# Kernel optimization log

Hardware: AMD Instinct MI355X
Metric: run time of the kernel (lower is better)

The kernel has to match this reference:

```python
import jax, jax.numpy as jnp
import numpy as np

B, A, IN, H, NA = 256, 32, 512, 512, 64


def setup_inputs() -> dict:
    key = jax.random.key(0)
    ks = jax.random.split(key, 9)
    s = 1.0 / np.sqrt(H).astype(np.float32)
    si = 1.0 / np.sqrt(IN).astype(np.float32)
    return {
        "inputs": jax.random.normal(ks[0], (B * A, IN), jnp.float32),
        "hidden_state": jnp.zeros((B, A, H), jnp.float32),
        "W1": jax.random.normal(ks[1], (A, H, IN), jnp.float32) * si,
        "b1": jax.random.normal(ks[2], (A, H), jnp.float32) * si,
        "W_ih": jax.random.normal(ks[3], (A, 3 * H, H), jnp.float32) * s,
        "b_ih": jax.random.normal(ks[4], (A, 3 * H), jnp.float32) * s,
        "W_hh": jax.random.normal(ks[5], (A, 3 * H, H), jnp.float32) * s,
        "b_hh": jax.random.normal(ks[6], (A, 3 * H), jnp.float32) * s,
        "W2": jax.random.normal(ks[7], (A, NA, H), jnp.float32) * s,
        "b2": jax.random.normal(ks[8], (A, NA), jnp.float32) * s,
    }


def reference(inputs, hidden_state, W1, b1, W_ih, b_ih, W_hh, b_hh, W2, b2):
    # inputs: [B*A, IN] -> [B, A, IN]; per-agent distinct weights stacked on axis 0 (a)
    x = inputs.reshape(-1, A, IN)
    h_in = hidden_state  # [B, A, H]
    # fc1 + relu, grouped over agents
    x1 = jax.nn.relu(jnp.einsum('bai,ahi->bah', x, W1) + b1)
    # GRUCell (PyTorch gate layout: r, z, n)
    gx = jnp.einsum('bah,agh->bag', x1, W_ih) + b_ih   # [B, A, 3H]
    gh = jnp.einsum('bah,agh->bag', h_in, W_hh) + b_hh  # [B, A, 3H]
    gx_r, gx_z, gx_n = jnp.split(gx, 3, axis=-1)
    gh_r, gh_z, gh_n = jnp.split(gh, 3, axis=-1)
    r = jax.nn.sigmoid(gx_r + gh_r)
    z = jax.nn.sigmoid(gx_z + gh_z)
    n = jnp.tanh(gx_n + r * gh_n)
    h = (1.0 - z) * n + z * h_in  # [B, A, H]
    # fc2 per agent
    q = jnp.einsum('bah,anh->ban', h, W2) + b2  # [B, A, NA]
    # torch: cat(qs, dim=-1).view(-1, n_actions) == reshape to [B*A, NA]
    return q.reshape(-1, NA), h
```

## Files before the change

kernel.cpp:

```cpp
#include <hip/hip_runtime.h>
#include <hip/hip_bf16.h>


typedef __attribute__((ext_vector_type(8))) __bf16 bf16x8;
typedef __attribute__((ext_vector_type(4))) float  f32x4;

constexpr int NAGENT = 32;
constexpr int KC     = 512;

__device__ __forceinline__ bf16x8 cvt8(const float* p) {
  f32x4 u = *(const f32x4*)p;
  f32x4 v = *(const f32x4*)(p + 4);
  bf16x8 w;
  w[0] = (__bf16)u[0]; w[1] = (__bf16)u[1]; w[2] = (__bf16)u[2]; w[3] = (__bf16)u[3];
  w[4] = (__bf16)v[0]; w[5] = (__bf16)v[1]; w[6] = (__bf16)v[2]; w[7] = (__bf16)v[3];
  return w;
}
__device__ __forceinline__ float sigmoid_f(float x) { return 1.f / (1.f + __expf(-x)); }
__device__ __forceinline__ float tanh_f(float x) {
  float xc = fminf(fmaxf(x, -15.f), 15.f);
  float a = __expf(2.f * xc);
  return (a - 1.f) / (a + 1.f);
}
__device__ __forceinline__ int xcd_swz(int bid, int nwg) {
  return (bid & 7) * (nwg >> 3) + (bid >> 3);
}


__global__ __launch_bounds__(256) void prep_k(
    const float* __restrict__ hidden, __bf16* __restrict__ AF) {
  const int idx = blockIdx.x * 256 + threadIdx.x;
  const int kc = idx & 63;
  const int row = idx >> 6;
  const int a = row & 31, b = row >> 5;
  bf16x8 v = cvt8(hidden + (size_t)row * KC + kc * 8);
  *(bf16x8*)(AF + ((size_t)(a * 128 + 64 + kc) * 256 + b) * 8) = v;
}

__global__ __launch_bounds__(512, 2) void fc1_k(
    const float* __restrict__ inputs, const float* __restrict__ W1,
    const float* __restrict__ b1, __bf16* __restrict__ AF) {
  const int wg = xcd_swz(blockIdx.x, gridDim.x);
  const int a  = wg >> 3;
  const int n0 = (wg & 7) * 64;

  __shared__ __attribute__((aligned(16))) __bf16 lA[2][256][8][8];
  __shared__ __attribute__((aligned(16))) __bf16 lB[2][64][8][8];

  const int tid = threadIdx.x;
  const int lane = tid & 63;
  const int wave = tid >> 6;
  const int wm = wave >> 1, wn = wave & 1;
  const int lr = lane & 15, lk = lane >> 4;

  int arow[4], aks[4]; size_t aoff[4];
#pragma unroll
  for (int c = 0; c < 4; ++c) {
    const int idx = c * 512 + tid;
    arow[c] = idx >> 3; aks[c] = idx & 7;
    aoff[c] = ((size_t)arow[c] * NAGENT + a) * KC + aks[c] * 8;
  }
  const int brow = tid >> 3, bks = tid & 7;
  const size_t boff = ((size_t)a * 512 + n0 + brow) * KC + bks * 8;

  bf16x8 sA[4], sB;
  auto loadT = [&](int t) {
    const int kb = t * 64;
#pragma unroll
    for (int c = 0; c < 4; ++c) sA[c] = cvt8(inputs + aoff[c] + kb);
    sB = cvt8(W1 + boff + kb);
  };
  auto writeT = [&](int buf) {
#pragma unroll
    for (int c = 0; c < 4; ++c)
      *(bf16x8*)(&lA[buf][arow[c]][aks[c] ^ (arow[c] & 7)][0]) = sA[c];
    *(bf16x8*)(&lB[buf][brow][bks ^ (brow & 7)][0]) = sB;
  };

  f32x4 acc[4][2] = {};
  auto computeT = [&](int buf) {
#pragma unroll
    for (int s = 0; s < 2; ++s) {
      const int ks = s * 4 + lk;
      bf16x8 af[4];
#pragma unroll
      for (int i = 0; i < 4; ++i) {
        const int row = wm * 64 + i * 16 + lr;
        af[i] = *(const bf16x8*)(&lA[buf][row][ks ^ (row & 7)][0]);
      }
#pragma unroll
      for (int cb = 0; cb < 2; ++cb) {
        const int br = wn * 32 + cb * 16 + lr;
        bf16x8 bv = *(const bf16x8*)(&lB[buf][br][ks ^ (br & 7)][0]);
#pragma unroll
        for (int i = 0; i < 4; ++i)
          acc[i][cb] = __builtin_amdgcn_mfma_f32_16x16x32_bf16(af[i], bv, acc[i][cb], 0, 0, 0);
      }
    }
  };

  loadT(0); writeT(0);
  int cur = 0;
#pragma unroll 1
  for (int t = 0; t < 8; ++t) {
    __syncthreads();
    if (t < 7) loadT(t + 1);
    computeT(cur);
    if (t < 7) { writeT(cur ^ 1); cur ^= 1; }
  }

#pragma unroll
  for (int cb = 0; cb < 2; ++cb) {
    const int col = n0 + wn * 32 + cb * 16 + lr;
    const int kc = col >> 3, c7 = col & 7;
    const float bias = b1[(size_t)a * 512 + col];
#pragma unroll
    for (int i = 0; i < 4; ++i) {
      const int r0 = wm * 64 + i * 16 + lk * 4;
#pragma unroll
      for (int e = 0; e < 4; ++e) {
        const float v = fmaxf(acc[i][cb][e] + bias, 0.f);
        AF[((size_t)(a * 128 + kc) * 256 + r0 + e) * 8 + c7] = (__bf16)v;
      }
    }
  }
}

__global__ __launch_bounds__(1024, 4) void gru_k(
    const __bf16* __restrict__ AF,
    const float* __restrict__ Wih, const float* __restrict__ bih,
    const float* __restrict__ Whh, const float* __restrict__ bhh,
    float* __restrict__ hout, __bf16* __restrict__ hbf) {
  const int wg = xcd_swz(blockIdx.x, gridDim.x);
  const int a  = wg >> 3;
  const int n0 = (wg & 7) * 64;

  __shared__ __attribute__((aligned(16))) __bf16 lB[2][192][8][8];

  const int tid = threadIdx.x;
  const int lane = tid & 63;
  const int wave = tid >> 6;
  const int wm = wave >> 1;
  const int wc = wave & 1;
  const int lr = lane & 15, lk = lane >> 4;

  const int br0 = tid >> 3, bks = tid & 7;
  const int br1 = 128 + (tid >> 3);
  auto wrow = [&](int r) {
    return (size_t)a * 1536 + (r >> 6) * 512 + n0 + (r & 63);
  };
  const size_t boff0 = wrow(br0) * KC + bks * 8;
  const size_t boff1 = (tid < 512 ? wrow(br1) * KC + bks * 8 : 0);

  size_t aBase[2];
#pragma unroll
  for (int i = 0; i < 2; ++i)
    aBase[i] = (size_t)a * 262144 + (size_t)lk * 2048 +
               (size_t)(wm * 32 + i * 16 + lr) * 8;

  bf16x8 sB0, sB1;
  auto loadB = [&](int t) {
    const float* W = (t < 8) ? Wih : Whh;
    const int kb = (t & 7) * 64;
    sB0 = cvt8(W + boff0 + kb);
    if (tid < 512) sB1 = cvt8(W + boff1 + kb);
  };
  auto writeB = [&](int buf) {
    *(bf16x8*)(&lB[buf][br0][bks ^ (br0 & 7)][0]) = sB0;
    if (tid < 512) *(bf16x8*)(&lB[buf][br1][bks ^ (br1 & 7)][0]) = sB1;
  };

  f32x4 accR[2][2] = {}, accZ[2][2] = {}, accXN[2][2] = {}, accHN[2][2] = {};
  auto compute = [&](int buf, int t, f32x4 (&accN)[2][2]) {
    bf16x8 af[2][2];
#pragma unroll
    for (int s = 0; s < 2; ++s)
#pragma unroll
      for (int i = 0; i < 2; ++i)
        af[s][i] = *(const bf16x8*)(AF + aBase[i] + (size_t)t * 16384 + s * 8192);
#pragma unroll
    for (int s = 0; s < 2; ++s) {
      const int ks = s * 4 + lk;
#pragma unroll
      for (int cc = 0; cc < 2; ++cc) {
        const int rr = wc * 32 + cc * 16 + lr;
        const int sw = ks ^ (rr & 7);
        bf16x8 bR = *(const bf16x8*)(&lB[buf][rr][sw][0]);
        bf16x8 bZ = *(const bf16x8*)(&lB[buf][64 + rr][sw][0]);
        bf16x8 bN = *(const bf16x8*)(&lB[buf][128 + rr][sw][0]);
#pragma unroll
        for (int i = 0; i < 2; ++i) {
          accR[i][cc] = __builtin_amdgcn_mfma_f32_16x16x32_bf16(af[s][i], bR, accR[i][cc], 0, 0, 0);
          accZ[i][cc] = __builtin_amdgcn_mfma_f32_16x16x32_bf16(af[s][i], bZ, accZ[i][cc], 0, 0, 0);
          accN[i][cc] = __builtin_amdgcn_mfma_f32_16x16x32_bf16(af[s][i], bN, accN[i][cc], 0, 0, 0);
        }
      }
    }
  };

  loadB(0); writeB(0);
  int cur = 0;
#pragma unroll 1
  for (int t = 0; t < 8; ++t) {
    __syncthreads();
    loadB(t + 1);
    compute(cur, t, accXN);
    writeB(cur ^ 1); cur ^= 1;
  }
#pragma unroll 1
  for (int t = 8; t < 16; ++t) {
    __syncthreads();
    if (t < 15) loadB(t + 1);
    compute(cur, t, accHN);
    if (t < 15) { writeB(cur ^ 1); cur ^= 1; }
  }

#pragma unroll
  for (int cc = 0; cc < 2; ++cc) {
    const int col = n0 + wc * 32 + cc * 16 + lr;
    const size_t ab = (size_t)a * 1536 + col;
    const float br_ = bih[ab] + bhh[ab];
    const float bz_ = bih[ab + 512] + bhh[ab + 512];
    const float bxn = bih[ab + 1024];
    const float bhn = bhh[ab + 1024];
    const size_t hfb = ((size_t)(a * 128 + 64 + (col >> 3)) * 256) * 8 + (col & 7);
#pragma unroll
    for (int i = 0; i < 2; ++i) {
      const int r0 = wm * 32 + i * 16 + lk * 4;
#pragma unroll
      for (int e = 0; e < 4; ++e) {
        const float hprev = (float)AF[hfb + (size_t)(r0 + e) * 8];
        const float r = sigmoid_f(accR[i][cc][e] + br_);
        const float z = sigmoid_f(accZ[i][cc][e] + bz_);
        const float n = tanh_f((accXN[i][cc][e] + bxn) + r * (accHN[i][cc][e] + bhn));
        const float h = (1.f - z) * n + z * hprev;
        const size_t o = ((size_t)(r0 + e) * NAGENT + a) * KC + col;
        hout[o] = h;
        hbf[o] = (__bf16)h;
      }
    }
  }
}

template <bool ABF16, int ACT, bool OBF16>
__global__ __launch_bounds__(256) void gemm64(
    const void* __restrict__ Ap, const float* __restrict__ Wp,
    const float* __restrict__ bp, void* __restrict__ Op, const int N) {
  constexpr int BM = 64, MT = 4;
  const int NT = N >> 6;
  const int wg = xcd_swz(blockIdx.x, gridDim.x);
  const int a  = wg / (MT * NT);
  const int rem = wg % (MT * NT);
  const int n0 = (rem / MT) * 64;
  const int b0 = (rem % MT) * BM;

  __shared__ __attribute__((aligned(16))) __bf16 lA[2][4][64][8];
  __shared__ __attribute__((aligned(16))) __bf16 lB[2][4][64][8];

  const int tid = threadIdx.x;
  const int lane = tid & 63;
  const int wn = tid >> 6;
  const int lr = lane & 15, lk = lane >> 4;

  const int ar = tid >> 2, aks = tid & 3;
  const size_t aoff = ((size_t)(b0 + ar) * NAGENT + a) * KC + aks * 8;
  const size_t boff = ((size_t)a * N + n0 + ar) * KC + aks * 8;

  const float*  Af = (const float*)Ap;
  const __bf16* Ab = (const __bf16*)Ap;

  bf16x8 sA, sB;
  auto loadT = [&](int t) {
    if constexpr (ABF16) sA = *(const bf16x8*)(Ab + aoff + t * 32);
    else                 sA = cvt8(Af + aoff + t * 32);
    sB = cvt8(Wp + boff + t * 32);
  };
  auto writeT = [&](int buf) {
    *(bf16x8*)(&lA[buf][aks][ar][0]) = sA;
    *(bf16x8*)(&lB[buf][aks][ar][0]) = sB;
  };

  f32x4 acc[4] = {};
  auto computeT = [&](int buf) {
    bf16x8 bv = *(const bf16x8*)(&lB[buf][lk][wn * 16 + lr][0]);
#pragma unroll
    for (int i = 0; i < 4; ++i) {
      bf16x8 af = *(const bf16x8*)(&lA[buf][lk][i * 16 + lr][0]);
      acc[i] = __builtin_amdgcn_mfma_f32_16x16x32_bf16(af, bv, acc[i], 0, 0, 0);
    }
  };

  loadT(0); writeT(0);
  int cur = 0;
#pragma unroll 1
  for (int t = 0; t < KC / 32; ++t) {
    __syncthreads();
    if (t + 1 < KC / 32) loadT(t + 1);
    computeT(cur);
    if (t + 1 < KC / 32) { writeT(cur ^ 1); cur ^= 1; }
  }

  const int col = n0 + wn * 16 + lr;
  const float bias = bp[(size_t)a * N + col];
#pragma unroll
  for (int i = 0; i < 4; ++i) {
    const int r0 = b0 + i * 16 + lk * 4;
#pragma unroll
    for (int e = 0; e < 4; ++e) {
      float v = acc[i][e] + bias;
      if (ACT == 1) v = fmaxf(v, 0.f);
      const size_t o = ((size_t)(r0 + e) * NAGENT + a) * N + col;
      if constexpr (OBF16) ((__bf16*)Op)[o] = (__bf16)v;
      else                 ((float*)Op)[o]  = v;
    }
  }
}

extern "C" void kernel_launch(void* const* d_in, const int* in_sizes, int n_in,
                              void* d_out, int out_size, void* d_ws, size_t ws_size,
                              hipStream_t stream) {
  const float* inputs = (const float*)d_in[0];
  const float* hidden = (const float*)d_in[1];
  const float* W1   = (const float*)d_in[2];
  const float* b1   = (const float*)d_in[3];
  const float* W_ih = (const float*)d_in[4];
  const float* b_ih = (const float*)d_in[5];
  const float* W_hh = (const float*)d_in[6];
  const float* b_hh = (const float*)d_in[7];
  const float* W2   = (const float*)d_in[8];
  const float* b2   = (const float*)d_in[9];

  float* out_q = (float*)d_out;
  float* out_h = out_q + (size_t)8192 * 64;

  char* ws = (char*)d_ws;
  __bf16* AF  = (__bf16*)(ws);
  __bf16* hbf = (__bf16*)(ws + ((size_t)16 << 20));

  prep_k<<<2048, 256, 0, stream>>>(hidden, AF);
  fc1_k<<<256, 512, 0, stream>>>(inputs, W1, b1, AF);
  gru_k<<<256, 1024, 0, stream>>>(AF, W_ih, b_ih, W_hh, b_hh, out_h, hbf);
  gemm64<true, 0, false><<<128, 256, 0, stream>>>(hbf, W2, b2, out_q, 64);
}
```

Before: 112.7 us.

## Deepen GRU gate GEMM pipeline with two-ahead B prefetch and A register double-buffer

The GRU gate GEMM loop now prefetches weight tiles two steps ahead into two register sets and double-buffers the A fragments in registers, loading the next step's A before computing the current one. The barrier moves to after the LDS write, and both loops are fully unrolled. The goal is to hide global-load latency behind MFMA work. In exchange it raises VGPR pressure, which may reduce occupancy, and the full unroll grows code size.

```diff
diff --git a/kernel.cpp b/kernel.cpp
--- a/kernel.cpp
+++ b/kernel.cpp
@@ -158,26 +158,29 @@
     aBase[i] = (size_t)a * 262144 + (size_t)lk * 2048 +
                (size_t)(wm * 32 + i * 16 + lr) * 8;
 
-  bf16x8 sB0, sB1;
-  auto loadB = [&](int t) {
+  bf16x8 sB[2][2];
+  auto loadB = [&](int t, int set) {
     const float* W = (t < 8) ? Wih : Whh;
     const int kb = (t & 7) * 64;
-    sB0 = cvt8(W + boff0 + kb);
-    if (tid < 512) sB1 = cvt8(W + boff1 + kb);
-  };
-  auto writeB = [&](int buf) {
-    *(bf16x8*)(&lB[buf][br0][bks ^ (br0 & 7)][0]) = sB0;
-    if (tid < 512) *(bf16x8*)(&lB[buf][br1][bks ^ (br1 & 7)][0]) = sB1;
+    sB[set][0] = cvt8(W + boff0 + kb);
+    if (tid < 512) sB[set][1] = cvt8(W + boff1 + kb);
+  };
+  auto writeB = [&](int buf, int set) {
+    *(bf16x8*)(&lB[buf][br0][bks ^ (br0 & 7)][0]) = sB[set][0];
+    if (tid < 512) *(bf16x8*)(&lB[buf][br1][bks ^ (br1 & 7)][0]) = sB[set][1];
+  };
+
+  bf16x8 afA[2][2], afB[2][2];
+  auto loadA = [&](bf16x8 (&dst)[2][2], int t) {
+#pragma unroll
+    for (int s = 0; s < 2; ++s)
+#pragma unroll
+      for (int i = 0; i < 2; ++i)
+        dst[s][i] = *(const bf16x8*)(AF + aBase[i] + (size_t)t * 16384 + s * 8192);
   };
 
   f32x4 accR[2][2] = {}, accZ[2][2] = {}, accXN[2][2] = {}, accHN[2][2] = {};
-  auto compute = [&](int buf, int t, f32x4 (&accN)[2][2]) {
-    bf16x8 af[2][2];
-#pragma unroll
-    for (int s = 0; s < 2; ++s)
-#pragma unroll
-      for (int i = 0; i < 2; ++i)
-        af[s][i] = *(const bf16x8*)(AF + aBase[i] + (size_t)t * 16384 + s * 8192);
+  auto compute = [&](int buf, bf16x8 (&af)[2][2], f32x4 (&accN)[2][2]) {
 #pragma unroll
     for (int s = 0; s < 2; ++s) {
       const int ks = s * 4 + lk;
@@ -198,22 +201,25 @@
     }
   };
 
-  loadB(0); writeB(0);
-  int cur = 0;
-#pragma unroll 1
-  for (int t = 0; t < 8; ++t) {
-    __syncthreads();
-    loadB(t + 1);
-    compute(cur, t, accXN);
-    writeB(cur ^ 1); cur ^= 1;
-  }
-#pragma unroll 1
-  for (int t = 8; t < 16; ++t) {
-    __syncthreads();
-    if (t < 15) loadB(t + 1);
-    compute(cur, t, accHN);
-    if (t < 15) { writeB(cur ^ 1); cur ^= 1; }
-  }
+  loadB(0, 0);
+  loadB(1, 1);
+  loadA(afA, 0);
+  writeB(0, 0);
+  __syncthreads();
+
+  auto step = [&](int t, f32x4 (&accN)[2][2]) {
+    const int nt = t + 1;
+    if (nt < 16) { if (t & 1) loadA(afA, nt); else loadA(afB, nt); }
+    if (t + 2 < 16) loadB(t + 2, t & 1);
+    if (t & 1) compute(1, afB, accN);
+    else       compute(0, afA, accN);
+    if (nt < 16) { writeB(nt & 1, nt & 1); __syncthreads(); }
+  };
+
+#pragma unroll
+  for (int t = 0; t < 8; ++t) step(t, accXN);
+#pragma unroll
+  for (int t = 8; t < 16; ++t) step(t, accHN);
 
 #pragma unroll
   for (int cc = 0; cc < 2; ++cc) {
```

After: 130.8 us. 16.1% more time.

## Prefetch A fragments into registers and fully unroll GRU GEMM main loop

Applied to the files above, without the earlier changes.

The GRU gate kernel now double-buffers the A-operand fragments in registers, loading step t+1 while step t's MFMAs run, rather than loading them at the start of each compute. Both K loops are fully unrolled with compile-time buffer indices. __syncthreads is replaced by an explicit lgkmcnt wait plus s_barrier and a sched_barrier. Index math drops from size_t to 32-bit ints. This aims to hide global-load latency and cut address arithmetic, at the cost of more VGPRs and a risk of spilling or lower occupancy.

```diff
diff --git a/kernel.cpp b/kernel.cpp
--- a/kernel.cpp
+++ b/kernel.cpp
@@ -24,6 +24,11 @@
 }
 __device__ __forceinline__ int xcd_swz(int bid, int nwg) {
   return (bid & 7) * (nwg >> 3) + (bid >> 3);
+}
+__device__ __forceinline__ void lds_barrier() {
+  asm volatile("s_waitcnt lgkmcnt(0)" ::: "memory");
+  __builtin_amdgcn_s_barrier();
+  __builtin_amdgcn_sched_barrier(0);
 }
 
 
@@ -145,18 +150,11 @@
   const int lr = lane & 15, lk = lane >> 4;
 
   const int br0 = tid >> 3, bks = tid & 7;
-  const int br1 = 128 + (tid >> 3);
-  auto wrow = [&](int r) {
-    return (size_t)a * 1536 + (r >> 6) * 512 + n0 + (r & 63);
-  };
-  const size_t boff0 = wrow(br0) * KC + bks * 8;
-  const size_t boff1 = (tid < 512 ? wrow(br1) * KC + bks * 8 : 0);
-
-  size_t aBase[2];
-#pragma unroll
-  for (int i = 0; i < 2; ++i)
-    aBase[i] = (size_t)a * 262144 + (size_t)lk * 2048 +
-               (size_t)(wm * 32 + i * 16 + lr) * 8;
+  const int br1 = 128 + br0;
+  const int boff0 = (a * 1536 + (br0 >> 6) * 512 + n0 + (br0 & 63)) * KC + bks * 8;
+  const int boff1 = (a * 1536 + (br1 >> 6) * 512 + n0 + (br1 & 63)) * KC + bks * 8;
+
+  const int aBase = a * 262144 + lk * 2048 + (wm * 32 + lr) * 8;
 
   bf16x8 sB0, sB1;
   auto loadB = [&](int t) {
@@ -170,14 +168,17 @@
     if (tid < 512) *(bf16x8*)(&lB[buf][br1][bks ^ (br1 & 7)][0]) = sB1;
   };
 
+  bf16x8 afA[2][2], afB[2][2];
+  auto loadA = [&](bf16x8 (&dst)[2][2], int t) {
+#pragma unroll
+    for (int s = 0; s < 2; ++s)
+#pragma unroll
+      for (int i = 0; i < 2; ++i)
+        dst[s][i] = *(const bf16x8*)(AF + aBase + t * 16384 + s * 8192 + i * 128);
+  };
+
   f32x4 accR[2][2] = {}, accZ[2][2] = {}, accXN[2][2] = {}, accHN[2][2] = {};
-  auto compute = [&](int buf, int t, f32x4 (&accN)[2][2]) {
-    bf16x8 af[2][2];
-#pragma unroll
-    for (int s = 0; s < 2; ++s)
-#pragma unroll
-      for (int i = 0; i < 2; ++i)
-        af[s][i] = *(const bf16x8*)(AF + aBase[i] + (size_t)t * 16384 + s * 8192);
+  auto compute = [&](int buf, bf16x8 (&af)[2][2], f32x4 (&accN)[2][2]) {
 #pragma unroll
     for (int s = 0; s < 2; ++s) {
       const int ks = s * 4 + lk;
@@ -198,21 +199,25 @@
     }
   };
 
-  loadB(0); writeB(0);
-  int cur = 0;
-#pragma unroll 1
+  loadB(0);
+  loadA(afA, 0);
+  writeB(0);
+  lds_barrier();
+
+#pragma unroll
   for (int t = 0; t < 8; ++t) {
-    __syncthreads();
     loadB(t + 1);
-    compute(cur, t, accXN);
-    writeB(cur ^ 1); cur ^= 1;
-  }
-#pragma unroll 1
+    if (t & 1) { loadA(afA, t + 1); compute(1, afB, accXN); }
+    else       { loadA(afB, t + 1); compute(0, afA, accXN); }
+    writeB((t + 1) & 1);
+    lds_barrier();
+  }
+#pragma unroll
   for (int t = 8; t < 16; ++t) {
-    __syncthreads();
     if (t < 15) loadB(t + 1);
-    compute(cur, t, accHN);
-    if (t < 15) { writeB(cur ^ 1); cur ^= 1; }
+    if (t & 1) { if (t < 15) loadA(afA, t + 1); compute(1, afB, accHN); }
+    else       { loadA(afB, t + 1);             compute(0, afA, accHN); }
+    if (t < 15) { writeB((t + 1) & 1); lds_barrier(); }
   }
 
 #pragma unroll
```

New measurement: 121.1 us. +7.5%, slower.
